# Performance work log

Hardware: AMD Instinct MI355X
Metric: run time of the kernel (lower is better)

The kernel has to match this reference:

```python
import jax, jax.numpy as jnp
import numpy as np

N_ENT = 100000
N_REL = 500
IN_DIM = 128
OUT_DIM = 128
E = 500000


def setup_inputs() -> dict:
    key = jax.random.key(0)
    ks = jax.random.split(key, 9)
    src = jax.random.randint(ks[0], (E,), 0, N_ENT)
    dst = jax.random.randint(ks[1], (E,), 0, N_ENT)
    rel = jax.random.randint(ks[2], (E,), 0, N_REL)
    ent_embed = jax.random.normal(ks[3], (N_ENT, IN_DIM), dtype=jnp.float32)
    rel_embed = jax.random.normal(ks[4], (N_REL, IN_DIM), dtype=jnp.float32)
    # xavier_normal with gain 1.414 for linear weights
    g = 1.414
    a_w = jax.random.normal(ks[5], (OUT_DIM, 3 * IN_DIM), dtype=jnp.float32) * (g * np.sqrt(2.0 / (3 * IN_DIM + OUT_DIM)))
    a_b = jnp.zeros((OUT_DIM,), dtype=jnp.float32)
    a2_w = jax.random.normal(ks[6], (1, OUT_DIM), dtype=jnp.float32) * (g * np.sqrt(2.0 / (OUT_DIM + 1)))
    a2_b = jnp.zeros((1,), dtype=jnp.float32)
    return {"ent_embed": ent_embed, "rel_embed": rel_embed, "a_w": a_w, "a_b": a_b,
            "a2_w": a2_w, "a2_b": a2_b, "src": src, "dst": dst, "rel": rel}


def reference(ent_embed, rel_embed, a_w, a_b, a2_w, a2_b, src, dst, rel):
    # gather: [E, 3*in_dim]
    h = jnp.concatenate([ent_embed[src], ent_embed[dst], rel_embed[rel]], axis=1)
    c = h @ a_w.T + a_b                      # [E, out_dim]
    b = jax.nn.leaky_relu(c @ a2_w.T + a2_b, negative_slope=0.01)  # [E, 1]
    e_b = jnp.exp(b)                          # [E, 1]
    temp1 = e_b * c                           # [E, out_dim]
    # scatter-sum into source nodes (SpecialSpmmFinal keyed on edges[0] = src)
    e_b_sum = jax.ops.segment_sum(e_b, src, num_segments=N_ENT)   # [N, 1]
    h_sum = jax.ops.segment_sum(temp1, src, num_segments=N_ENT)   # [N, out_dim]
    ebs = jnp.where(e_b_sum == 0, jnp.float32(1e-12), e_b_sum)
    h_ent = h_sum / ebs
    # scatter-mean of temp1 by relation id
    rel_sum = jax.ops.segment_sum(temp1, rel, num_segments=N_REL)          # [R, out_dim]
    rel_cnt = jax.ops.segment_sum(jnp.ones((temp1.shape[0],), jnp.float32), rel, num_segments=N_REL)
    h_rel = rel_sum / jnp.maximum(rel_cnt, 1.0)[:, None]
    return (jax.nn.elu(h_ent), jax.nn.elu(h_rel))
```

## Files before the change

### kernel.cpp

```cpp
#include <hip/hip_runtime.h>
#include <hip/hip_bf16.h>

#define N_ENT_C 100000
#define N_REL_C 500
#define NEDGE_C 500000
#define SCAN_BLOCKS 391
#define EPB 1024
#define NB_EDGE 489
#define CHUNK_B 62

#define OFF_WTHI  0
#define OFF_WTLO  16384
#define OFF_WTR   32768
#define OFF_PR    49152
#define OFF_PRH   113152
#define OFF_STAGE 145152
#define OFF_PSH   1445760
#define OFF_PDH   7845760

#define DO_OSRC     0
#define DO_DSTS     100000
#define DO_RELS     600000
#define DO_QS       1100000
#define DO_QD       1200000
#define DO_QR       1300000
#define SCRATCH_ROWS 10161
#define DO_HSRC     1300512
#define DO_BSUM     1400512
#define DO_RELSTART 1401024
#define DO_PART8    1401536
#define DO_CHUNKOFF 1405632
#define DO_BLKHIST  1409728
#define DO_BLKOFFS  1660096
#define DO_SRCR     1910464
#define DO_DSTR     2410464
#define DO_RELP     2910464

typedef short bf16x8 __attribute__((ext_vector_type(8)));
typedef short s16x4  __attribute__((ext_vector_type(4)));
typedef float f32x4  __attribute__((ext_vector_type(4)));
typedef unsigned short u16x8 __attribute__((ext_vector_type(8)));

__device__ inline unsigned short bf_rne(float x) {
    unsigned int u = __float_as_uint(x);
    u += 0x7FFF + ((u >> 16) & 1);
    return (unsigned short)(u >> 16);
}
__device__ inline float bf2f(unsigned short h) {
    return __uint_as_float(((unsigned int)h) << 16);
}

__global__ void prep_w(const float* __restrict__ aw, unsigned short* __restrict__ Wthi,
                       unsigned short* __restrict__ Wtlo, float* __restrict__ Wtr) {
    int idx = blockIdx.x * 256 + threadIdx.x;
    if (idx < 32768) {
        int n = idx >> 7, k = idx & 127;
        float v = (n < 128) ? aw[n * 384 + k] : aw[(n - 128) * 384 + 128 + k];
        unsigned short h = bf_rne(v);
        Wthi[idx] = h;
        Wtlo[idx] = bf_rne(v - bf2f(h));
    } else if (idx < 49152) {
        int t = idx - 32768;
        int k = t >> 7, o = t & 127;
        Wtr[t] = aw[o * 384 + 256 + k];
    }
}

__global__ void rel_proj(const float* __restrict__ rele, const float* __restrict__ Wtr,
                         const float* __restrict__ ab, const float* __restrict__ a2w,
                         float* __restrict__ Pr, unsigned short* __restrict__ PrH,
                         float* __restrict__ qr) {
    int r = blockIdx.x;
    int o = threadIdx.x;
    float acc = ab[o];
    for (int k = 0; k < 128; ++k)
        acc = fmaf(rele[r * 128 + k], Wtr[k * 128 + o], acc);
    Pr[r * 128 + o] = acc;
    PrH[r * 128 + o] = bf_rne(acc);
    __shared__ float red[128];
    red[o] = acc * a2w[o];
    __syncthreads();
    for (int off = 64; off > 0; off >>= 1) {
        if (o < off) red[o] += red[o + off];
        __syncthreads();
    }
    if (o == 0) qr[r] = red[0];
}

__global__ __launch_bounds__(256) void ent_mfma(const float* __restrict__ ent,
                                                const unsigned short* __restrict__ Wthi,
                                                const unsigned short* __restrict__ Wtlo,
                                                const float* __restrict__ a2w,
                                                unsigned short* __restrict__ PsH,
                                                unsigned short* __restrict__ PdH,
                                                float* __restrict__ qs,
                                                float* __restrict__ qd) {
    __shared__ __align__(16) char sh[32768];
    __shared__ float qred[4][64];
    const int tid = threadIdx.x;
    const int block_row = blockIdx.x * 64;

#pragma unroll
    for (int i = 0; i < 8; ++i) {
        int f = tid + i * 256;
        int m = f >> 5, k4 = f & 31;
        float4 v = make_float4(0.f, 0.f, 0.f, 0.f);
        int grow = block_row + m;
        if (grow < N_ENT_C) v = *(const float4*)&ent[(size_t)grow * 128 + k4 * 4];
        unsigned short h0 = bf_rne(v.x), h1 = bf_rne(v.y), h2 = bf_rne(v.z), h3 = bf_rne(v.w);
        s16x4 hv; hv[0] = (short)h0; hv[1] = (short)h1; hv[2] = (short)h2; hv[3] = (short)h3;
        s16x4 lv;
        lv[0] = (short)bf_rne(v.x - bf2f(h0));
        lv[1] = (short)bf_rne(v.y - bf2f(h1));
        lv[2] = (short)bf_rne(v.z - bf2f(h2));
        lv[3] = (short)bf_rne(v.w - bf2f(h3));
        int off = m * 256 + k4 * 8;
        off ^= (m & 7) << 4;
        *(s16x4*)(sh + off) = hv;
        *(s16x4*)(sh + 16384 + off) = lv;
    }
    __syncthreads();

    const int w = tid >> 6, lane = tid & 63;
    const int l15 = lane & 15, lh = lane >> 4;
    const int n0 = w * 64;

    f32x4 zz = {0.f, 0.f, 0.f, 0.f};
    f32x4 acc[4][4];
#pragma unroll
    for (int mf = 0; mf < 4; ++mf)
#pragma unroll
        for (int nf = 0; nf < 4; ++nf) acc[mf][nf] = zz;

#pragma unroll
    for (int ks = 0; ks < 4; ++ks) {
        int kb = ks * 32 + lh * 8;
        bf16x8 ah[4], al[4];
#pragma unroll
        for (int mf = 0; mf < 4; ++mf) {
            int row = mf * 16 + l15;
            int off = row * 256 + kb * 2;
            off ^= (row & 7) << 4;
            ah[mf] = *(const bf16x8*)(sh + off);
            al[mf] = *(const bf16x8*)(sh + 16384 + off);
        }
#pragma unroll
        for (int nf = 0; nf < 4; ++nf) {
            int n = n0 + nf * 16 + l15;
            bf16x8 bh = *(const bf16x8*)(Wthi + n * 128 + kb);
            bf16x8 bl = *(const bf16x8*)(Wtlo + n * 128 + kb);
#pragma unroll
            for (int mf = 0; mf < 4; ++mf) {
                acc[mf][nf] = __builtin_amdgcn_mfma_f32_16x16x32_bf16(ah[mf], bh, acc[mf][nf], 0, 0, 0);
                acc[mf][nf] = __builtin_amdgcn_mfma_f32_16x16x32_bf16(ah[mf], bl, acc[mf][nf], 0, 0, 0);
                acc[mf][nf] = __builtin_amdgcn_mfma_f32_16x16x32_bf16(al[mf], bh, acc[mf][nf], 0, 0, 0);
            }
        }
    }

    float a2[4];
#pragma unroll
    for (int nf = 0; nf < 4; ++nf) a2[nf] = a2w[(n0 + nf * 16 + l15) & 127];
    float qp[4][4];
#pragma unroll
    for (int mf = 0; mf < 4; ++mf)
#pragma unroll
        for (int v = 0; v < 4; ++v) qp[mf][v] = 0.f;

#pragma unroll
    for (int mf = 0; mf < 4; ++mf) {
#pragma unroll
        for (int nf = 0; nf < 4; ++nf) {
            int col = n0 + nf * 16 + l15;
#pragma unroll
            for (int v = 0; v < 4; ++v) {
                float val = acc[mf][nf][v];
                qp[mf][v] = fmaf(val, a2[nf], qp[mf][v]);
                int row = block_row + mf * 16 + lh * 4 + v;
                if (row < N_ENT_C) {
                    unsigned short hv = bf_rne(val);
                    if (col < 128) PsH[(size_t)row * 128 + col] = hv;
                    else PdH[(size_t)row * 128 + (col - 128)] = hv;
                }
            }
        }
    }
#pragma unroll
    for (int mf = 0; mf < 4; ++mf)
#pragma unroll
        for (int v = 0; v < 4; ++v) {
            float q = qp[mf][v];
            q += __shfl_xor(q, 1);
            q += __shfl_xor(q, 2);
            q += __shfl_xor(q, 4);
            q += __shfl_xor(q, 8);
            qp[mf][v] = q;
        }
    if (l15 == 0) {
#pragma unroll
        for (int mf = 0; mf < 4; ++mf)
#pragma unroll
            for (int v = 0; v < 4; ++v) qred[w][mf * 16 + lh * 4 + v] = qp[mf][v];
    }
    __syncthreads();
    if (tid < 64) {
        int row = block_row + tid;
        if (row < N_ENT_C) {
            qs[row] = qred[0][tid] + qred[1][tid];
            qd[row] = qred[2][tid] + qred[3][tid];
        }
    }
}

__global__ __launch_bounds__(256) void edge_hist(const int* __restrict__ src,
                                                 const int* __restrict__ rel,
                                                 int* __restrict__ histSrc,
                                                 int* __restrict__ blkHist) {
    __shared__ int lh[512];
    int tid = threadIdx.x;
    lh[tid] = 0; lh[tid + 256] = 0;
    __syncthreads();
    int base = blockIdx.x * EPB;
#pragma unroll
    for (int j = 0; j < 4; ++j) {
        int e = base + j * 256 + tid;
        if (e < NEDGE_C) {
            atomicAdd(&histSrc[src[e]], 1);
            atomicAdd(&lh[rel[e]], 1);
        }
    }
    __syncthreads();
    blkHist[blockIdx.x * 512 + tid] = lh[tid];
    blkHist[blockIdx.x * 512 + 256 + tid] = lh[tid + 256];
}

__global__ void colsum(const int* __restrict__ blkHist, int* __restrict__ partial) {
    int r = threadIdx.x;
    int k = blockIdx.x;
    int b0 = k * CHUNK_B;
    int b1 = min(b0 + CHUNK_B, NB_EDGE);
    int t = 0;
    for (int b = b0; b < b1; ++b) t += blkHist[b * 512 + r];
    partial[k * 512 + r] = t;
}

__global__ void scan512(const int* __restrict__ partial, int* __restrict__ relStart,
                        int* __restrict__ chunkOff) {
    __shared__ int a[512], b2[512];
    int tid = threadIdx.x;
    int p8[8];
    int t = 0;
#pragma unroll
    for (int k = 0; k < 8; ++k) { p8[k] = partial[k * 512 + tid]; t += p8[k]; }
    a[tid] = t;
    __syncthreads();
    int v = t;
    int* cur = a; int* nxt = b2;
    for (int off = 1; off < 512; off <<= 1) {
        int x = cur[tid] + ((tid >= off) ? cur[tid - off] : 0);
        nxt[tid] = x;
        __syncthreads();
        int* tmp = cur; cur = nxt; nxt = tmp;
    }
    int excl = cur[tid] - v;
    relStart[tid] = excl;
    int run = excl;
#pragma unroll
    for (int k = 0; k < 8; ++k) { chunkOff[k * 512 + tid] = run; run += p8[k]; }
}

__global__ void colscan(const int* __restrict__ blkHist, const int* __restrict__ chunkOff,
                        int* __restrict__ blockOffs) {
    int r = threadIdx.x;
    int k = blockIdx.x;
    int b0 = k * CHUNK_B;
    int b1 = min(b0 + CHUNK_B, NB_EDGE);
    int off = chunkOff[k * 512 + r];
    for (int b = b0; b < b1; ++b) {
        blockOffs[b * 512 + r] = off;
        off += blkHist[b * 512 + r];
    }
}

__global__ void scan_blockred(const int* __restrict__ hist, int* __restrict__ blockSums, int n) {
    __shared__ int s[256];
    int tid = threadIdx.x;
    int i = blockIdx.x * 256 + tid;
    s[tid] = (i < n) ? hist[i] : 0;
    __syncthreads();
    for (int off = 128; off > 0; off >>= 1) {
        if (tid < off) s[tid] += s[tid + off];
        __syncthreads();
    }
    if (tid == 0) blockSums[blockIdx.x] = s[0];
}

__global__ void scan_single(int* __restrict__ data, int n) {
    __shared__ int a[1024], b2[1024];
    int tid = threadIdx.x;
    int v = (tid < n) ? data[tid] : 0;
    a[tid] = v;
    __syncthreads();
    int* cur = a; int* nxt = b2;
    for (int off = 1; off < 1024; off <<= 1) {
        int x = cur[tid] + ((tid >= off) ? cur[tid - off] : 0);
        nxt[tid] = x;
        __syncthreads();
        int* t = cur; cur = nxt; nxt = t;
    }
    if (tid < n) data[tid] = cur[tid] - v;
}

__global__ void scan_final(const int* __restrict__ hist, const int* __restrict__ blockOffs,
                           int* __restrict__ offs, int n) {
    __shared__ int a[256], b2[256];
    int tid = threadIdx.x;
    int i = blockIdx.x * 256 + tid;
    int v = (i < n) ? hist[i] : 0;
    a[tid] = v;
    __syncthreads();
    int* cur = a; int* nxt = b2;
    for (int off = 1; off < 256; off <<= 1) {
        int x = cur[tid] + ((tid >= off) ? cur[tid - off] : 0);
        nxt[tid] = x;
        __syncthreads();
        int* t = cur; cur = nxt; nxt = t;
    }
    if (i < n) offs[i] = cur[tid] - v + blockOffs[blockIdx.x];
}

__global__ __launch_bounds__(256) void scatter_both(const int* __restrict__ src,
                                                    const int* __restrict__ dst,
                                                    const int* __restrict__ rel,
                                                    int* __restrict__ offsSrc,
                                                    const int* __restrict__ blockOffs,
                                                    int* __restrict__ dstS, int* __restrict__ relS,
                                                    int* __restrict__ srcR, int* __restrict__ dstR) {
    __shared__ int lh[512];
    int tid = threadIdx.x;
    lh[tid] = 0; lh[tid + 256] = 0;
    __syncthreads();
    int base = blockIdx.x * EPB;
    const int* bo = &blockOffs[blockIdx.x * 512];
#pragma unroll
    for (int j = 0; j < 4; ++j) {
        int e = base + j * 256 + tid;
        if (e < NEDGE_C) {
            int s = src[e], d = dst[e], r = rel[e];
            int p = atomicAdd(&offsSrc[s], 1);
            dstS[p] = d; relS[p] = r;
            int lr = atomicAdd(&lh[r], 1);
            int q = bo[r] + lr;
            srcR[q] = s; dstR[q] = d;
        }
    }
}

__global__ __launch_bounds__(256) void rel_phase(const unsigned short* __restrict__ PsH,
                                                 const unsigned short* __restrict__ PdH,
                                                 const float* __restrict__ qs,
                                                 const float* __restrict__ qd,
                                                 const float* __restrict__ qr,
                                                 const int* __restrict__ relStart,
                                                 const int* __restrict__ srcR,
                                                 const int* __restrict__ dstR,
                                                 const float* __restrict__ a2b,
                                                 float* __restrict__ relpart) {
    int r = blockIdx.x >> 3;
    int p = blockIdx.x & 7;
    int start = relStart[r];
    int end = relStart[r + 1];
    int tid = threadIdx.x;
    int w = tid >> 6;
    int h = (tid >> 5) & 1;
    int l = tid & 31;
    int slot = p * 8 + w * 2 + h;
    float bb = a2b[0];
    float qrr = qr[r];
    float4 acc = make_float4(0.f, 0.f, 0.f, 0.f);
    float ebs = 0.f;
    for (int i = start + slot; i < end; i += 64) {
        int s = srcR[i], d = dstR[i];
        float b = qs[s] + qd[d] + qrr + bb;
        b = (b > 0.f) ? b : 0.01f * b;
        float eb = expf(b);
        ushort4 pv = *(const ushort4*)&PsH[(size_t)s * 128 + l * 4];
        ushort4 dv = *(const ushort4*)&PdH[(size_t)d * 128 + l * 4];
        acc.x = fmaf(eb, bf2f(pv.x) + bf2f(dv.x), acc.x);
        acc.y = fmaf(eb, bf2f(pv.y) + bf2f(dv.y), acc.y);
        acc.z = fmaf(eb, bf2f(pv.z) + bf2f(dv.z), acc.z);
        acc.w = fmaf(eb, bf2f(pv.w) + bf2f(dv.w), acc.w);
        ebs += eb;
    }
    __shared__ float vred[8][128];
    __shared__ float sred[8];
    int sub = w * 2 + h;
    *(float4*)&vred[sub][l * 4] = acc;
    if (l == 0) sred[sub] = ebs;
    __syncthreads();
    if (tid < 128) {
        float v = 0.f;
#pragma unroll
        for (int k2 = 0; k2 < 8; ++k2) v += vred[k2][tid];
        float e = 0.f;
#pragma unroll
        for (int k2 = 0; k2 < 8; ++k2) e += sred[k2];
        int pi = r * 8 + p;
        relpart[pi * 132 + tid] = v;
        if (tid == 0) relpart[pi * 132 + 128] = e;
    }
}

__global__ void rel_fin(const float* __restrict__ relpart, const float* __restrict__ Pr,
                        const int* __restrict__ relStart, float* __restrict__ outRel) {
    int r = blockIdx.x;
    int o = threadIdx.x;
    float v = 0.f, e = 0.f;
#pragma unroll
    for (int p = 0; p < 8; ++p) {
        v += relpart[(r * 8 + p) * 132 + o];
        e += relpart[(r * 8 + p) * 132 + 128];
    }
    float cnt = (float)(relStart[r + 1] - relStart[r]);
    float h = (v + e * Pr[r * 128 + o]) / fmaxf(cnt, 1.f);
    outRel[r * 128 + o] = (h > 0.f) ? h : (expf(h) - 1.f);
}

__global__ __launch_bounds__(256) void src_phase(const unsigned short* __restrict__ PsH,
                                                 const unsigned short* __restrict__ PdH,
                                                 const unsigned short* __restrict__ PrH,
                                                 const float* __restrict__ qs,
                                                 const float* __restrict__ qd,
                                                 const float* __restrict__ qr,
                                                 const int* __restrict__ offsSrc,
                                                 const int* __restrict__ dstS,
                                                 const int* __restrict__ relS,
                                                 const float* __restrict__ a2b,
                                                 float* __restrict__ stage,
                                                 float* __restrict__ out) {
    int wid = (blockIdx.x * 256 + threadIdx.x) >> 6;
    if (wid >= N_ENT_C) return;
    int lane = threadIdx.x & 63;
    int g = lane >> 4, l = lane & 15;
    int s = wid;
    int start = (s == 0) ? 0 : offsSrc[s - 1];
    int end = offsSrc[s];
    float* dstp = (s < SCRATCH_ROWS) ? &stage[(size_t)s * 128] : &out[(size_t)s * 128];
    if (end == start) {
        if (g == 0) {
            *(float4*)&dstp[l * 8] = make_float4(0.f, 0.f, 0.f, 0.f);
            *(float4*)&dstp[l * 8 + 4] = make_float4(0.f, 0.f, 0.f, 0.f);
        }
        return;
    }
    float bb = a2b[0];
    float qss = qs[s];
    float acc[8];
#pragma unroll
    for (int j = 0; j < 8; ++j) acc[j] = 0.f;
    float ebs = 0.f;
    for (int i = start + g; i < end; i += 4) {
        int d = dstS[i], r = relS[i];
        float b = qss + qd[d] + qr[r] + bb;
        b = (b > 0.f) ? b : 0.01f * b;
        float eb = expf(b);
        u16x8 dv = *(const u16x8*)&PdH[(size_t)d * 128 + l * 8];
        u16x8 rv = *(const u16x8*)&PrH[(size_t)r * 128 + l * 8];
#pragma unroll
        for (int j = 0; j < 8; ++j)
            acc[j] = fmaf(eb, bf2f(dv[j]) + bf2f(rv[j]), acc[j]);
        ebs += eb;
    }
#pragma unroll
    for (int j = 0; j < 8; ++j) {
        acc[j] += __shfl_xor(acc[j], 16);
        acc[j] += __shfl_xor(acc[j], 32);
    }
    ebs += __shfl_xor(ebs, 16);
    ebs += __shfl_xor(ebs, 32);
    if (g == 0) {
        float inv = 1.f / ebs;
        u16x8 ps = *(const u16x8*)&PsH[(size_t)s * 128 + l * 8];
        float h[8];
#pragma unroll
        for (int j = 0; j < 8; ++j) {
            float x = bf2f(ps[j]) + acc[j] * inv;
            h[j] = (x > 0.f) ? x : (expf(x) - 1.f);
        }
        *(float4*)&dstp[l * 8]     = make_float4(h[0], h[1], h[2], h[3]);
        *(float4*)&dstp[l * 8 + 4] = make_float4(h[4], h[5], h[6], h[7]);
    }
}

extern "C" void kernel_launch(void* const* d_in, const int* in_sizes, int n_in,
                              void* d_out, int out_size, void* d_ws, size_t ws_size,
                              hipStream_t stream) {
    const float* ent  = (const float*)d_in[0];
    const float* rele = (const float*)d_in[1];
    const float* aw   = (const float*)d_in[2];
    const float* ab   = (const float*)d_in[3];
    const float* a2w  = (const float*)d_in[4];
    const float* a2b  = (const float*)d_in[5];
    const int* src    = (const int*)d_in[6];
    const int* dst    = (const int*)d_in[7];
    const int* rel    = (const int*)d_in[8];
    float* out = (float*)d_out;

    float* ws = (float*)d_ws;
    unsigned short* Wthi = (unsigned short*)(ws + OFF_WTHI);
    unsigned short* Wtlo = (unsigned short*)(ws + OFF_WTLO);
    float* Wtr = ws + OFF_WTR;
    float* Pr  = ws + OFF_PR;
    unsigned short* PrH = (unsigned short*)(ws + OFF_PRH);
    float* stage = ws + OFF_STAGE;
    unsigned short* PsH = (unsigned short*)(ws + OFF_PSH);
    unsigned short* PdH = (unsigned short*)(ws + OFF_PDH);

    int* dI = (int*)d_out;
    int* offsSrc  = dI + DO_OSRC;
    int* dstS     = dI + DO_DSTS;
    int* relS     = dI + DO_RELS;
    float* qs     = (float*)dI + DO_QS;
    float* qd     = (float*)dI + DO_QD;
    float* qr     = (float*)dI + DO_QR;
    int* histSrc  = dI + DO_HSRC;
    int* bsum     = dI + DO_BSUM;
    int* relStart = dI + DO_RELSTART;
    int* part8    = dI + DO_PART8;
    int* chunkOff = dI + DO_CHUNKOFF;
    int* blkHist  = dI + DO_BLKHIST;
    int* blockOffs= dI + DO_BLKOFFS;
    int* srcR     = dI + DO_SRCR;
    int* dstR     = dI + DO_DSTR;
    float* relpart = (float*)dI + DO_RELP;

    hipMemsetAsync(histSrc, 0, (size_t)N_ENT_C * sizeof(int), stream);

    prep_w<<<192, 256, 0, stream>>>(aw, Wthi, Wtlo, Wtr);
    rel_proj<<<N_REL_C, 128, 0, stream>>>(rele, Wtr, ab, a2w, Pr, PrH, qr);
    ent_mfma<<<(N_ENT_C + 63) / 64, 256, 0, stream>>>(ent, Wthi, Wtlo, a2w, PsH, PdH, qs, qd);

    edge_hist<<<NB_EDGE, 256, 0, stream>>>(src, rel, histSrc, blkHist);
    colsum<<<8, 512, 0, stream>>>(blkHist, part8);
    scan512<<<1, 512, 0, stream>>>(part8, relStart, chunkOff);
    colscan<<<8, 512, 0, stream>>>(blkHist, chunkOff, blockOffs);
    scan_blockred<<<SCAN_BLOCKS, 256, 0, stream>>>(histSrc, bsum, N_ENT_C);
    scan_single<<<1, 1024, 0, stream>>>(bsum, SCAN_BLOCKS);
    scan_final<<<SCAN_BLOCKS, 256, 0, stream>>>(histSrc, bsum, offsSrc, N_ENT_C);
    scatter_both<<<NB_EDGE, 256, 0, stream>>>(src, dst, rel, offsSrc, blockOffs,
                                              dstS, relS, srcR, dstR);

    rel_phase<<<N_REL_C * 8, 256, 0, stream>>>(PsH, PdH, qs, qd, qr, relStart, srcR, dstR,
                                               a2b, relpart);
    rel_fin<<<N_REL_C, 128, 0, stream>>>(relpart, Pr, relStart, out + (size_t)N_ENT_C * 128);

    src_phase<<<(N_ENT_C + 3) / 4, 256, 0, stream>>>(PsH, PdH, PrH, qs, qd, qr,
                                                     offsSrc, dstS, relS, a2b, stage, out);

    hipMemcpyAsync(out, stage, (size_t)SCRATCH_ROWS * 128 * sizeof(float),
                   hipMemcpyDeviceToDevice, stream);
}
```

Baseline: 269.3 us.

## Make entity projection persistent with register-resident weights and atomic score accumulation

The entity projection kernel becomes persistent: 1250 blocks loop over 16-row tiles. Each wave loads its slice of the split-bf16 weights into registers once, instead of staging entity rows through LDS and re-reading weights for every block. The MFMA operands are swapped so each lane holds four consecutive output columns, which allows vectorized ushort4 stores. The per-row attention partial sums are reduced with shuffles and added to qs/qd atomically, which needs a widened memset to zero those buffers first. This trades LDS traffic and barriers for heavy register pressure (launch bounds of 2) and float atomics.

```diff
diff --git a/kernel.cpp b/kernel.cpp
--- a/kernel.cpp
+++ b/kernel.cpp
@@ -8,6 +8,8 @@
 #define EPB 1024
 #define NB_EDGE 489
 #define CHUNK_B 62
+#define MT_TOTAL 6250
+#define ENT_GRID 1250
 
 #define OFF_WTHI  0
 #define OFF_WTLO  16384
@@ -37,7 +39,6 @@
 #define DO_RELP     2910464
 
 typedef short bf16x8 __attribute__((ext_vector_type(8)));
-typedef short s16x4  __attribute__((ext_vector_type(4)));
 typedef float f32x4  __attribute__((ext_vector_type(4)));
 typedef unsigned short u16x8 __attribute__((ext_vector_type(8)));
 
@@ -87,128 +88,90 @@
     if (o == 0) qr[r] = red[0];
 }
 
-__global__ __launch_bounds__(256) void ent_mfma(const float* __restrict__ ent,
-                                                const unsigned short* __restrict__ Wthi,
-                                                const unsigned short* __restrict__ Wtlo,
-                                                const float* __restrict__ a2w,
-                                                unsigned short* __restrict__ PsH,
-                                                unsigned short* __restrict__ PdH,
-                                                float* __restrict__ qs,
-                                                float* __restrict__ qd) {
-    __shared__ __align__(16) char sh[32768];
-    __shared__ float qred[4][64];
+__global__ __launch_bounds__(256, 2) void ent_mfma(const float* __restrict__ ent,
+                                                   const unsigned short* __restrict__ Wthi,
+                                                   const unsigned short* __restrict__ Wtlo,
+                                                   const float* __restrict__ a2w,
+                                                   unsigned short* __restrict__ PsH,
+                                                   unsigned short* __restrict__ PdH,
+                                                   float* __restrict__ qs,
+                                                   float* __restrict__ qd) {
     const int tid = threadIdx.x;
-    const int block_row = blockIdx.x * 64;
-
-#pragma unroll
-    for (int i = 0; i < 8; ++i) {
-        int f = tid + i * 256;
-        int m = f >> 5, k4 = f & 31;
-        float4 v = make_float4(0.f, 0.f, 0.f, 0.f);
-        int grow = block_row + m;
-        if (grow < N_ENT_C) v = *(const float4*)&ent[(size_t)grow * 128 + k4 * 4];
-        unsigned short h0 = bf_rne(v.x), h1 = bf_rne(v.y), h2 = bf_rne(v.z), h3 = bf_rne(v.w);
-        s16x4 hv; hv[0] = (short)h0; hv[1] = (short)h1; hv[2] = (short)h2; hv[3] = (short)h3;
-        s16x4 lv;
-        lv[0] = (short)bf_rne(v.x - bf2f(h0));
-        lv[1] = (short)bf_rne(v.y - bf2f(h1));
-        lv[2] = (short)bf_rne(v.z - bf2f(h2));
-        lv[3] = (short)bf_rne(v.w - bf2f(h3));
-        int off = m * 256 + k4 * 8;
-        off ^= (m & 7) << 4;
-        *(s16x4*)(sh + off) = hv;
-        *(s16x4*)(sh + 16384 + off) = lv;
-    }
-    __syncthreads();
-
     const int w = tid >> 6, lane = tid & 63;
     const int l15 = lane & 15, lh = lane >> 4;
     const int n0 = w * 64;
 
+    bf16x8 wh[4][4], wl[4][4];
+#pragma unroll
+    for (int nf = 0; nf < 4; ++nf) {
+        int n = n0 + nf * 16 + l15;
+#pragma unroll
+        for (int ks = 0; ks < 4; ++ks) {
+            int kb = ks * 32 + lh * 8;
+            wh[nf][ks] = *(const bf16x8*)(Wthi + n * 128 + kb);
+            wl[nf][ks] = *(const bf16x8*)(Wtlo + n * 128 + kb);
+        }
+    }
+    float a2v[4][4];
+#pragma unroll
+    for (int nf = 0; nf < 4; ++nf)
+#pragma unroll
+        for (int v = 0; v < 4; ++v)
+            a2v[nf][v] = a2w[(n0 + nf * 16 + lh * 4 + v) & 127];
+
+    const bool isPs = (w < 2);
+    unsigned short* PH = isPs ? PsH : PdH;
+    float* qout = isPs ? qs : qd;
+    const int colbase0 = (n0 & 127) + lh * 4;
+
     f32x4 zz = {0.f, 0.f, 0.f, 0.f};
-    f32x4 acc[4][4];
-#pragma unroll
-    for (int mf = 0; mf < 4; ++mf)
-#pragma unroll
-        for (int nf = 0; nf < 4; ++nf) acc[mf][nf] = zz;
-
-#pragma unroll
-    for (int ks = 0; ks < 4; ++ks) {
-        int kb = ks * 32 + lh * 8;
-        bf16x8 ah[4], al[4];
-#pragma unroll
-        for (int mf = 0; mf < 4; ++mf) {
-            int row = mf * 16 + l15;
-            int off = row * 256 + kb * 2;
-            off ^= (row & 7) << 4;
-            ah[mf] = *(const bf16x8*)(sh + off);
-            al[mf] = *(const bf16x8*)(sh + 16384 + off);
-        }
+
+    for (int mt = blockIdx.x; mt < MT_TOTAL; mt += ENT_GRID) {
+        const int m = mt * 16 + l15;
+        bf16x8 eh[4], el[4];
+#pragma unroll
+        for (int ks = 0; ks < 4; ++ks) {
+            int kb = ks * 32 + lh * 8;
+            float4 e0 = *(const float4*)&ent[(size_t)m * 128 + kb];
+            float4 e1 = *(const float4*)&ent[(size_t)m * 128 + kb + 4];
+            float f[8] = {e0.x, e0.y, e0.z, e0.w, e1.x, e1.y, e1.z, e1.w};
+            bf16x8 hv, lv;
+#pragma unroll
+            for (int j = 0; j < 8; ++j) {
+                unsigned short h = bf_rne(f[j]);
+                hv[j] = (short)h;
+                lv[j] = (short)bf_rne(f[j] - bf2f(h));
+            }
+            eh[ks] = hv; el[ks] = lv;
+        }
+
+        f32x4 acc[4];
+#pragma unroll
+        for (int nf = 0; nf < 4; ++nf) acc[nf] = zz;
+#pragma unroll
+        for (int ks = 0; ks < 4; ++ks)
+#pragma unroll
+            for (int nf = 0; nf < 4; ++nf) {
+                acc[nf] = __builtin_amdgcn_mfma_f32_16x16x32_bf16(wh[nf][ks], eh[ks], acc[nf], 0, 0, 0);
+                acc[nf] = __builtin_amdgcn_mfma_f32_16x16x32_bf16(wh[nf][ks], el[ks], acc[nf], 0, 0, 0);
+                acc[nf] = __builtin_amdgcn_mfma_f32_16x16x32_bf16(wl[nf][ks], eh[ks], acc[nf], 0, 0, 0);
+            }
+
+        float qp = 0.f;
 #pragma unroll
         for (int nf = 0; nf < 4; ++nf) {
-            int n = n0 + nf * 16 + l15;
-            bf16x8 bh = *(const bf16x8*)(Wthi + n * 128 + kb);
-            bf16x8 bl = *(const bf16x8*)(Wtlo + n * 128 + kb);
-#pragma unroll
-            for (int mf = 0; mf < 4; ++mf) {
-                acc[mf][nf] = __builtin_amdgcn_mfma_f32_16x16x32_bf16(ah[mf], bh, acc[mf][nf], 0, 0, 0);
-                acc[mf][nf] = __builtin_amdgcn_mfma_f32_16x16x32_bf16(ah[mf], bl, acc[mf][nf], 0, 0, 0);
-                acc[mf][nf] = __builtin_amdgcn_mfma_f32_16x16x32_bf16(al[mf], bh, acc[mf][nf], 0, 0, 0);
-            }
-        }
-    }
-
-    float a2[4];
-#pragma unroll
-    for (int nf = 0; nf < 4; ++nf) a2[nf] = a2w[(n0 + nf * 16 + l15) & 127];
-    float qp[4][4];
-#pragma unroll
-    for (int mf = 0; mf < 4; ++mf)
-#pragma unroll
-        for (int v = 0; v < 4; ++v) qp[mf][v] = 0.f;
-
-#pragma unroll
-    for (int mf = 0; mf < 4; ++mf) {
-#pragma unroll
-        for (int nf = 0; nf < 4; ++nf) {
-            int col = n0 + nf * 16 + l15;
-#pragma unroll
-            for (int v = 0; v < 4; ++v) {
-                float val = acc[mf][nf][v];
-                qp[mf][v] = fmaf(val, a2[nf], qp[mf][v]);
-                int row = block_row + mf * 16 + lh * 4 + v;
-                if (row < N_ENT_C) {
-                    unsigned short hv = bf_rne(val);
-                    if (col < 128) PsH[(size_t)row * 128 + col] = hv;
-                    else PdH[(size_t)row * 128 + (col - 128)] = hv;
-                }
-            }
-        }
-    }
-#pragma unroll
-    for (int mf = 0; mf < 4; ++mf)
-#pragma unroll
-        for (int v = 0; v < 4; ++v) {
-            float q = qp[mf][v];
-            q += __shfl_xor(q, 1);
-            q += __shfl_xor(q, 2);
-            q += __shfl_xor(q, 4);
-            q += __shfl_xor(q, 8);
-            qp[mf][v] = q;
-        }
-    if (l15 == 0) {
-#pragma unroll
-        for (int mf = 0; mf < 4; ++mf)
-#pragma unroll
-            for (int v = 0; v < 4; ++v) qred[w][mf * 16 + lh * 4 + v] = qp[mf][v];
-    }
-    __syncthreads();
-    if (tid < 64) {
-        int row = block_row + tid;
-        if (row < N_ENT_C) {
-            qs[row] = qred[0][tid] + qred[1][tid];
-            qd[row] = qred[2][tid] + qred[3][tid];
-        }
+            ushort4 st;
+            st.x = bf_rne(acc[nf][0]);
+            st.y = bf_rne(acc[nf][1]);
+            st.z = bf_rne(acc[nf][2]);
+            st.w = bf_rne(acc[nf][3]);
+#pragma unroll
+            for (int v = 0; v < 4; ++v) qp = fmaf(acc[nf][v], a2v[nf][v], qp);
+            *(ushort4*)&PH[(size_t)m * 128 + colbase0 + nf * 16] = st;
+        }
+        qp += __shfl_xor(qp, 16);
+        qp += __shfl_xor(qp, 32);
+        if (lane < 16) unsafeAtomicAdd(&qout[m], qp);
     }
 }
 
@@ -534,11 +497,11 @@
     int* dstR     = dI + DO_DSTR;
     float* relpart = (float*)dI + DO_RELP;
 
-    hipMemsetAsync(histSrc, 0, (size_t)N_ENT_C * sizeof(int), stream);
+    hipMemsetAsync(dI + DO_QS, 0, (size_t)(DO_HSRC + N_ENT_C - DO_QS) * sizeof(int), stream);
 
     prep_w<<<192, 256, 0, stream>>>(aw, Wthi, Wtlo, Wtr);
     rel_proj<<<N_REL_C, 128, 0, stream>>>(rele, Wtr, ab, a2w, Pr, PrH, qr);
-    ent_mfma<<<(N_ENT_C + 63) / 64, 256, 0, stream>>>(ent, Wthi, Wtlo, a2w, PsH, PdH, qs, qd);
+    ent_mfma<<<ENT_GRID, 256, 0, stream>>>(ent, Wthi, Wtlo, a2w, PsH, PdH, qs, qd);
 
     edge_hist<<<NB_EDGE, 256, 0, stream>>>(src, rel, histSrc, blkHist);
     colsum<<<8, 512, 0, stream>>>(blkHist, part8);
```

Measured after the change: 265.5 us. No clear change (-1.4%).
